# Performance work log

Measured on AMD Instinct MI355X. Metric: run time of the kernel, lower is better.

## Reference

```python
import jax, jax.numpy as jnp
import numpy as np
from jax import lax

KS = 3
N = KS * KS


def _conv(x, W, b, pad, stride):
    out = lax.conv_general_dilated(
        x, W, window_strides=(stride, stride),
        padding=[(pad, pad), (pad, pad)],
        dimension_numbers=("NCHW", "OIHW", "NCHW"))
    return out + b[None, :, None, None]


def setup_inputs() -> dict:
    key = jax.random.key(0)
    ks = jax.random.split(key, 5)
    b, c, h, w, outc = 16, 64, 64, 64, 128
    return {
        "x": jax.random.normal(ks[0], (b, c, h, w), jnp.float32),
        "W_off": jax.random.normal(ks[1], (2 * N, c, KS, KS), jnp.float32) * 0.05,
        "b_off": jax.random.normal(ks[2], (2 * N,), jnp.float32) * 0.05,
        "W_k": jax.random.normal(ks[3], (outc, c, KS, KS), jnp.float32) * 0.05,
        "b_k": jax.random.normal(ks[4], (outc,), jnp.float32) * 0.05,
    }


def _deform_conv(x, W_off, b_off, W_k, b_k):
    b, c, h, w = x.shape
    offset = _conv(x, W_off, b_off, pad=1, stride=1)  # [b, 2N, h, w]

    # kernel-grid offsets, flattened with x (row) index first: n = i*ks + j
    rng = jnp.arange(KS, dtype=x.dtype) - (KS - 1) // 2  # [-1, 0, 1]
    pnx = jnp.repeat(rng, KS)  # [N]
    pny = jnp.tile(rng, KS)    # [N]

    # sampling positions p = p0 + p_n + offset, clamped into the image
    px = jnp.arange(h, dtype=x.dtype)[None, None, :, None] + pnx[None, :, None, None] + offset[:, :N]
    py = jnp.arange(w, dtype=x.dtype)[None, None, None, :] + pny[None, :, None, None] + offset[:, N:]
    px = jnp.clip(px, 0, h - 1)
    py = jnp.clip(py, 0, w - 1)

    fx = jnp.floor(px)
    fy = jnp.floor(py)
    tx = px - fx  # fractional parts (bilinear weights)
    ty = py - fy
    x0 = fx.astype(jnp.int32)
    y0 = fy.astype(jnp.int32)
    x1 = jnp.minimum(x0 + 1, h - 1)  # out-of-range tap carries zero weight
    y1 = jnp.minimum(y0 + 1, w - 1)

    x_hw = x.transpose(0, 2, 3, 1).reshape(b, h * w, c)  # [b, hw, c]

    def gather(ix, iy):
        idx = (ix * w + iy).reshape(b, -1, 1)  # [b, N*h*w, 1]
        return jnp.take_along_axis(x_hw, idx, axis=1).reshape(b, N, h, w, c)

    wx0, wx1 = (1 - tx)[..., None], tx[..., None]
    wy0, wy1 = (1 - ty)[..., None], ty[..., None]
    # 4-tap bilinear interpolation == the original's sparse G @ x
    xo = (gather(x0, y0) * wx0 * wy0 + gather(x1, y0) * wx1 * wy0
          + gather(x0, y1) * wx0 * wy1 + gather(x1, y1) * wx1 * wy1)  # [b,N,h,w,c]

    # _reshape_x_offset: out[b,c, i_h*ks+i, i_w*ks+j] = xo[b, i*ks+j, i_h, i_w, c]
    xo = xo.reshape(b, KS, KS, h, w, c).transpose(0, 5, 3, 1, 4, 2)
    xo = xo.reshape(b, c, h * KS, w * KS)

    return _conv(xo, W_k, b_k, pad=0, stride=KS)  # [b, outc, h, w]


def reference(x, W_off, b_off, W_k, b_k):
    return _deform_conv(x, W_off, b_off, W_k, b_k)
```

## Files before the change

### kernel.cpp

```cpp
#include <hip/hip_runtime.h>

typedef __attribute__((ext_vector_type(8))) short bf16x8;
typedef __attribute__((ext_vector_type(4))) float floatx4;

__device__ __forceinline__ unsigned short f2bf(float f) {
    unsigned int u = __float_as_uint(f);
    u += 0x7FFFu + ((u >> 16) & 1u);
    return (unsigned short)(u >> 16);
}

__global__ __launch_bounds__(256) void prep_all(const float* __restrict__ x,
        const float* __restrict__ Wk, const float* __restrict__ Woff,
        unsigned short* __restrict__ xt, unsigned short* __restrict__ Wkb2,
        unsigned short* __restrict__ Woffb) {
    int bb = blockIdx.x;
    if (bb < 1024) {
        __shared__ float tile[64][65];
        int b = bb >> 6, y = bb & 63;
        const float* src = x + (size_t)b * 262144 + y * 64;
        int tx = threadIdx.x & 15, tg = threadIdx.x >> 4;
#pragma unroll
        for (int i = 0; i < 4; i++) {
            int c = tg + i * 16;
            float4 v = *(const float4*)(src + (size_t)c * 4096 + tx * 4);
            tile[c][tx * 4 + 0] = v.x; tile[c][tx * 4 + 1] = v.y;
            tile[c][tx * 4 + 2] = v.z; tile[c][tx * 4 + 3] = v.w;
        }
        __syncthreads();
        unsigned short* dst = xt + (size_t)bb * 4096;
#pragma unroll
        for (int i = 0; i < 4; i++) {
            int xc = tg + i * 16;
            int c4 = tx * 4;
            ushort4 v;
            v.x = f2bf(tile[c4 + 0][xc]); v.y = f2bf(tile[c4 + 1][xc]);
            v.z = f2bf(tile[c4 + 2][xc]); v.w = f2bf(tile[c4 + 3][xc]);
            *(ushort4*)(dst + xc * 64 + c4) = v;
        }
    } else if (bb < 1312) {
        int idx = (bb - 1024) * 256 + threadIdx.x;
        int tap = idx >> 13;
        int r = idx & 8191;
        int tile = r >> 9;
        int ln = (r >> 3) & 63;
        int j = r & 7;
        int mt = tile >> 1, kc = tile & 1;
        int oc = mt * 16 + (ln & 15);
        int c = kc * 32 + (ln >> 4) * 8 + j;
        Wkb2[idx] = f2bf(Wk[(oc * 64 + c) * 9 + tap]);
    } else {
        int idx = (bb - 1312) * 256 + threadIdx.x;
        int tap = idx >> 11;
        int r = idx & 2047;
        int tile = r >> 9;
        int ln = (r >> 3) & 63;
        int j = r & 7;
        int mt = tile >> 1, kc = tile & 1;
        int n = mt * 16 + (ln & 15);
        int c = kc * 32 + (ln >> 4) * 8 + j;
        float v = (n < 18) ? Woff[(n * 64 + c) * 9 + tap] : 0.f;
        Woffb[idx] = f2bf(v);
    }
}

__global__ __launch_bounds__(256, 4) void fused_kernel(
        const unsigned short* __restrict__ xt,
        const unsigned short* __restrict__ Wkb2,
        const unsigned short* __restrict__ Woffb,
        const float* __restrict__ boff,
        const float* __restrict__ bias,
        float* __restrict__ out) {
    __shared__ unsigned short As[2][8192];
    __shared__ float offs[64][20];
    int tid = threadIdx.x;
    int wave = tid >> 6, lane = tid & 63;
    int frow = lane & 15, quad = lane >> 4;
    int bb = blockIdx.x;
    int xcd = bb & 7, idx = bb >> 3;
    int b = xcd * 2 + (idx >> 6);
    int pxBase = (idx & 63) * 64;
    int pl = wave * 16 + frow;
    int px = pxBase + pl;
    int y = px >> 6, xx = px & 63;
    const char* img = (const char*)(xt + (size_t)b * 262144) + quad * 16;

    float bv[2][4];
#pragma unroll
    for (int mt = 0; mt < 2; mt++)
#pragma unroll
        for (int rg = 0; rg < 4; rg++) {
            int n = mt * 16 + quad * 4 + rg;
            bv[mt][rg] = (n < 18) ? boff[n] : 0.f;
        }

    floatx4 acc1[2];
    acc1[0] = (floatx4)(0.f); acc1[1] = (floatx4)(0.f);
    bf16x8 aw = *(const bf16x8*)(Woffb + tid * 8);
    *(bf16x8*)&As[0][tid * 8] = aw;
    for (int tap = 0; tap < 9; tap++) {
        if (tap < 8) aw = *(const bf16x8*)(Woffb + (tap + 1) * 2048 + tid * 8);
        __syncthreads();
        int ry = y + tap / 3 - 1, rx = xx + tap % 3 - 1;
        bool valid = (ry >= 0) & (ry < 64) & (rx >= 0) & (rx < 64);
        const char* src = img + ((ry * 64 + rx) << 7);
        const unsigned short* abuf = &As[tap & 1][0];
        bf16x8 bz = {};
#pragma unroll
        for (int kc = 0; kc < 2; kc++) {
            bf16x8 bfr = valid ? *(const bf16x8*)(src + kc * 64) : bz;
#pragma unroll
            for (int mt = 0; mt < 2; mt++) {
                bf16x8 af = *(const bf16x8*)&abuf[(mt * 2 + kc) * 512 + lane * 8];
                acc1[mt] = __builtin_amdgcn_mfma_f32_16x16x32_bf16(af, bfr, acc1[mt], 0, 0, 0);
            }
        }
        if (tap < 8) *(bf16x8*)&As[(tap + 1) & 1][tid * 8] = aw;
    }
#pragma unroll
    for (int mt = 0; mt < 2; mt++)
#pragma unroll
        for (int rg = 0; rg < 4; rg++) {
            int n = mt * 16 + quad * 4 + rg;
            if (n < 18) offs[pl][n] = acc1[mt][rg] + bv[mt][rg];
        }

    floatx4 acc[8];
#pragma unroll
    for (int i = 0; i < 8; i++) acc[i] = (floatx4)(0.f);
    bf16x8 wk[4];
#pragma unroll
    for (int i = 0; i < 4; i++)
        wk[i] = *(const bf16x8*)(Wkb2 + i * 2048 + tid * 8);
    __syncthreads();
#pragma unroll
    for (int i = 0; i < 4; i++)
        *(bf16x8*)&As[0][i * 2048 + tid * 8] = wk[i];

    for (int tap = 0; tap < 9; tap++) {
        if (tap < 8)
#pragma unroll
            for (int i = 0; i < 4; i++)
                wk[i] = *(const bf16x8*)(Wkb2 + (tap + 1) * 8192 + i * 2048 + tid * 8);
        __syncthreads();
        float orow = offs[pl][tap];
        float ocol = offs[pl][9 + tap];
        float pr = (float)(y + tap / 3 - 1) + orow;
        float pc = (float)(xx + tap % 3 - 1) + ocol;
        pr = fminf(fmaxf(pr, 0.f), 63.f);
        pc = fminf(fmaxf(pc, 0.f), 63.f);
        float fr = floorf(pr), fc = floorf(pc);
        float tr = pr - fr, tc = pc - fc;
        int r0 = (int)fr, c0 = (int)fc;
        int r1 = min(r0 + 1, 63), c1 = min(c0 + 1, 63);
        float w00 = (1.f - tr) * (1.f - tc);
        float w01 = (1.f - tr) * tc;
        float w10 = tr * (1.f - tc);
        float w11 = tr * tc;
        int o00 = (r0 * 64 + c0) * 128;
        int o01 = (r0 * 64 + c1) * 128;
        int o10 = (r1 * 64 + c0) * 128;
        int o11 = (r1 * 64 + c1) * 128;

        bf16x8 bfrag[2];
#pragma unroll
        for (int kc = 0; kc < 2; kc++) {
            int4 u00 = __builtin_bit_cast(int4, *(const bf16x8*)(img + o00 + kc * 64));
            int4 u01 = __builtin_bit_cast(int4, *(const bf16x8*)(img + o01 + kc * 64));
            int4 u10 = __builtin_bit_cast(int4, *(const bf16x8*)(img + o10 + kc * 64));
            int4 u11 = __builtin_bit_cast(int4, *(const bf16x8*)(img + o11 + kc * 64));
            int4 r;
#pragma unroll
            for (int wd = 0; wd < 4; wd++) {
                int a00 = (wd == 0) ? u00.x : (wd == 1) ? u00.y : (wd == 2) ? u00.z : u00.w;
                int a01 = (wd == 0) ? u01.x : (wd == 1) ? u01.y : (wd == 2) ? u01.z : u01.w;
                int a10 = (wd == 0) ? u10.x : (wd == 1) ? u10.y : (wd == 2) ? u10.z : u10.w;
                int a11 = (wd == 0) ? u11.x : (wd == 1) ? u11.y : (wd == 2) ? u11.z : u11.w;
                float vl = w00 * __uint_as_float((unsigned)a00 << 16)
                         + w01 * __uint_as_float((unsigned)a01 << 16)
                         + w10 * __uint_as_float((unsigned)a10 << 16)
                         + w11 * __uint_as_float((unsigned)a11 << 16);
                float vh = w00 * __uint_as_float((unsigned)a00 & 0xffff0000u)
                         + w01 * __uint_as_float((unsigned)a01 & 0xffff0000u)
                         + w10 * __uint_as_float((unsigned)a10 & 0xffff0000u)
                         + w11 * __uint_as_float((unsigned)a11 & 0xffff0000u);
                unsigned pk = __builtin_amdgcn_perm(
                    __float_as_uint(vh) + 0x8000u,
                    __float_as_uint(vl) + 0x8000u, 0x07060302u);
                if (wd == 0) r.x = (int)pk; else if (wd == 1) r.y = (int)pk;
                else if (wd == 2) r.z = (int)pk; else r.w = (int)pk;
            }
            bfrag[kc] = __builtin_bit_cast(bf16x8, r);
        }
        const unsigned short* abuf = &As[tap & 1][0];
#pragma unroll
        for (int kc = 0; kc < 2; kc++)
#pragma unroll
            for (int mt = 0; mt < 8; mt++) {
                bf16x8 af = *(const bf16x8*)&abuf[(mt * 2 + kc) * 512 + lane * 8];
                acc[mt] = __builtin_amdgcn_mfma_f32_16x16x32_bf16(af, bfrag[kc], acc[mt], 0, 0, 0);
            }
        if (tap < 8)
#pragma unroll
            for (int i = 0; i < 4; i++)
                *(bf16x8*)&As[(tap + 1) & 1][i * 2048 + tid * 8] = wk[i];
    }

    float* outb = out + (size_t)b * 524288 + px;
#pragma unroll
    for (int mt = 0; mt < 8; mt++) {
#pragma unroll
        for (int rg = 0; rg < 4; rg++) {
            int oc = mt * 16 + quad * 4 + rg;
            outb[oc * 4096] = acc[mt][rg] + bias[oc];
        }
    }
}

extern "C" void kernel_launch(void* const* d_in, const int* in_sizes, int n_in,
                              void* d_out, int out_size, void* d_ws, size_t ws_size,
                              hipStream_t stream) {
    const float* x    = (const float*)d_in[0];
    const float* Woff = (const float*)d_in[1];
    const float* boff = (const float*)d_in[2];
    const float* Wk   = (const float*)d_in[3];
    const float* bk   = (const float*)d_in[4];
    float* out = (float*)d_out;

    char* ws = (char*)d_ws;
    unsigned short* xt    = (unsigned short*)ws;
    unsigned short* Wkb2  = (unsigned short*)(ws + 8388608);
    unsigned short* Woffb = (unsigned short*)(ws + 8536064);

    prep_all<<<1384, 256, 0, stream>>>(x, Wk, Woff, xt, Wkb2, Woffb);
    fused_kernel<<<1024, 256, 0, stream>>>(xt, Wkb2, Woffb, boff, bk, out);
}
```

Before: 132.1 us.

## Drop LDS weight staging, read weights from global, and prefetch next-tap gathers

Removes the shared-memory double buffer for the offset-conv and main-conv weights. Each wave now loads its weight fragments directly from global/L2, which also removes the per-tap block barriers. The four bilinear corner loads for the next tap are issued before the current tap's interpolation and MFMAs, so gather latency overlaps compute. The cost is more redundant global weight traffic (every wave reloads the same weights) and higher register pressure from holding prefetched corners and weight fragments, which could hurt occupancy.

```diff
diff --git a/kernel.cpp b/kernel.cpp
--- a/kernel.cpp
+++ b/kernel.cpp
@@ -7,6 +7,20 @@
     unsigned int u = __float_as_uint(f);
     u += 0x7FFFu + ((u >> 16) & 1u);
     return (unsigned short)(u >> 16);
+}
+
+__device__ __forceinline__ int interp_word(int a00, int a01, int a10, int a11,
+                                           float w00, float w01, float w10, float w11) {
+    float vl = w00 * __uint_as_float((unsigned)a00 << 16)
+             + w01 * __uint_as_float((unsigned)a01 << 16)
+             + w10 * __uint_as_float((unsigned)a10 << 16)
+             + w11 * __uint_as_float((unsigned)a11 << 16);
+    float vh = w00 * __uint_as_float((unsigned)a00 & 0xffff0000u)
+             + w01 * __uint_as_float((unsigned)a01 & 0xffff0000u)
+             + w10 * __uint_as_float((unsigned)a10 & 0xffff0000u)
+             + w11 * __uint_as_float((unsigned)a11 & 0xffff0000u);
+    return (int)__builtin_amdgcn_perm(__float_as_uint(vh) + 0x8000u,
+                                      __float_as_uint(vl) + 0x8000u, 0x07060302u);
 }
 
 __global__ __launch_bounds__(256) void prep_all(const float* __restrict__ x,
@@ -70,7 +84,6 @@
         const float* __restrict__ boff,
         const float* __restrict__ bias,
         float* __restrict__ out) {
-    __shared__ unsigned short As[2][8192];
     __shared__ float offs[64][20];
     int tid = threadIdx.x;
     int wave = tid >> 6, lane = tid & 63;
@@ -95,26 +108,22 @@
 
     floatx4 acc1[2];
     acc1[0] = (floatx4)(0.f); acc1[1] = (floatx4)(0.f);
-    bf16x8 aw = *(const bf16x8*)(Woffb + tid * 8);
-    *(bf16x8*)&As[0][tid * 8] = aw;
+#pragma unroll
     for (int tap = 0; tap < 9; tap++) {
-        if (tap < 8) aw = *(const bf16x8*)(Woffb + (tap + 1) * 2048 + tid * 8);
-        __syncthreads();
         int ry = y + tap / 3 - 1, rx = xx + tap % 3 - 1;
         bool valid = (ry >= 0) & (ry < 64) & (rx >= 0) & (rx < 64);
         const char* src = img + ((ry * 64 + rx) << 7);
-        const unsigned short* abuf = &As[tap & 1][0];
+        const unsigned short* wofft = Woffb + tap * 2048 + lane * 8;
         bf16x8 bz = {};
 #pragma unroll
         for (int kc = 0; kc < 2; kc++) {
             bf16x8 bfr = valid ? *(const bf16x8*)(src + kc * 64) : bz;
 #pragma unroll
             for (int mt = 0; mt < 2; mt++) {
-                bf16x8 af = *(const bf16x8*)&abuf[(mt * 2 + kc) * 512 + lane * 8];
+                bf16x8 af = *(const bf16x8*)(wofft + (mt * 2 + kc) * 512);
                 acc1[mt] = __builtin_amdgcn_mfma_f32_16x16x32_bf16(af, bfr, acc1[mt], 0, 0, 0);
             }
         }
-        if (tap < 8) *(bf16x8*)&As[(tap + 1) & 1][tid * 8] = aw;
     }
 #pragma unroll
     for (int mt = 0; mt < 2; mt++)
@@ -123,27 +132,18 @@
             int n = mt * 16 + quad * 4 + rg;
             if (n < 18) offs[pl][n] = acc1[mt][rg] + bv[mt][rg];
         }
+    __syncthreads();
 
     floatx4 acc[8];
 #pragma unroll
     for (int i = 0; i < 8; i++) acc[i] = (floatx4)(0.f);
-    bf16x8 wk[4];
-#pragma unroll
-    for (int i = 0; i < 4; i++)
-        wk[i] = *(const bf16x8*)(Wkb2 + i * 2048 + tid * 8);
-    __syncthreads();
-#pragma unroll
-    for (int i = 0; i < 4; i++)
-        *(bf16x8*)&As[0][i * 2048 + tid * 8] = wk[i];
-
-    for (int tap = 0; tap < 9; tap++) {
-        if (tap < 8)
-#pragma unroll
-            for (int i = 0; i < 4; i++)
-                wk[i] = *(const bf16x8*)(Wkb2 + (tap + 1) * 8192 + i * 2048 + tid * 8);
-        __syncthreads();
-        float orow = offs[pl][tap];
-        float ocol = offs[pl][9 + tap];
+
+    const float* op = &offs[pl][0];
+
+    auto stage = [&](int tap, int4 (&r00)[2], int4 (&r01)[2], int4 (&r10)[2],
+                     int4 (&r11)[2], floatx4& w) {
+        float orow = op[tap];
+        float ocol = op[9 + tap];
         float pr = (float)(y + tap / 3 - 1) + orow;
         float pc = (float)(xx + tap % 3 - 1) + ocol;
         pr = fminf(fmaxf(pr, 0.f), 63.f);
@@ -152,66 +152,87 @@
         float tr = pr - fr, tc = pc - fc;
         int r0 = (int)fr, c0 = (int)fc;
         int r1 = min(r0 + 1, 63), c1 = min(c0 + 1, 63);
-        float w00 = (1.f - tr) * (1.f - tc);
-        float w01 = (1.f - tr) * tc;
-        float w10 = tr * (1.f - tc);
-        float w11 = tr * tc;
-        int o00 = (r0 * 64 + c0) * 128;
-        int o01 = (r0 * 64 + c1) * 128;
-        int o10 = (r1 * 64 + c0) * 128;
-        int o11 = (r1 * 64 + c1) * 128;
+        w[0] = (1.f - tr) * (1.f - tc);
+        w[1] = (1.f - tr) * tc;
+        w[2] = tr * (1.f - tc);
+        w[3] = tr * tc;
+        const char* p00 = img + ((r0 * 64 + c0) << 7);
+        const char* p01 = img + ((r0 * 64 + c1) << 7);
+        const char* p10 = img + ((r1 * 64 + c0) << 7);
+        const char* p11 = img + ((r1 * 64 + c1) << 7);
+#pragma unroll
+        for (int kc = 0; kc < 2; kc++) {
+            r00[kc] = *(const int4*)(p00 + kc * 64);
+            r01[kc] = *(const int4*)(p01 + kc * 64);
+            r10[kc] = *(const int4*)(p10 + kc * 64);
+            r11[kc] = *(const int4*)(p11 + kc * 64);
+        }
+    };
+
+    int4 c00[2], c01[2], c10[2], c11[2];
+    floatx4 cw;
+    stage(0, c00, c01, c10, c11, cw);
+
+#pragma unroll 1
+    for (int tap = 0; tap < 9; tap++) {
+        const unsigned short* wkt = Wkb2 + tap * 8192 + lane * 8;
+
+        bf16x8 af0[8];
+#pragma unroll
+        for (int mt = 0; mt < 8; mt++)
+            af0[mt] = *(const bf16x8*)(wkt + (mt * 2) * 512);
+
+        int4 n00[2], n01[2], n10[2], n11[2];
+        floatx4 nw;
+        if (tap < 8)
+            stage(tap + 1, n00, n01, n10, n11, nw);
 
         bf16x8 bfrag[2];
 #pragma unroll
         for (int kc = 0; kc < 2; kc++) {
-            int4 u00 = __builtin_bit_cast(int4, *(const bf16x8*)(img + o00 + kc * 64));
-            int4 u01 = __builtin_bit_cast(int4, *(const bf16x8*)(img + o01 + kc * 64));
-            int4 u10 = __builtin_bit_cast(int4, *(const bf16x8*)(img + o10 + kc * 64));
-            int4 u11 = __builtin_bit_cast(int4, *(const bf16x8*)(img + o11 + kc * 64));
             int4 r;
-#pragma unroll
-            for (int wd = 0; wd < 4; wd++) {
-                int a00 = (wd == 0) ? u00.x : (wd == 1) ? u00.y : (wd == 2) ? u00.z : u00.w;
-                int a01 = (wd == 0) ? u01.x : (wd == 1) ? u01.y : (wd == 2) ? u01.z : u01.w;
-                int a10 = (wd == 0) ? u10.x : (wd == 1) ? u10.y : (wd == 2) ? u10.z : u10.w;
-                int a11 = (wd == 0) ? u11.x : (wd == 1) ? u11.y : (wd == 2) ? u11.z : u11.w;
-                float vl = w00 * __uint_as_float((unsigned)a00 << 16)
-                         + w01 * __uint_as_float((unsigned)a01 << 16)
-                         + w10 * __uint_as_float((unsigned)a10 << 16)
-                         + w11 * __uint_as_float((unsigned)a11 << 16);
-                float vh = w00 * __uint_as_float((unsigned)a00 & 0xffff0000u)
-                         + w01 * __uint_as_float((unsigned)a01 & 0xffff0000u)
-                         + w10 * __uint_as_float((unsigned)a10 & 0xffff0000u)
-                         + w11 * __uint_as_float((unsigned)a11 & 0xffff0000u);
-                unsigned pk = __builtin_amdgcn_perm(
-                    __float_as_uint(vh) + 0x8000u,
-                    __float_as_uint(vl) + 0x8000u, 0x07060302u);
-                if (wd == 0) r.x = (int)pk; else if (wd == 1) r.y = (int)pk;
-                else if (wd == 2) r.z = (int)pk; else r.w = (int)pk;
+            r.x = interp_word(c00[kc].x, c01[kc].x, c10[kc].x, c11[kc].x,
+                              cw[0], cw[1], cw[2], cw[3]);
+            r.y = interp_word(c00[kc].y, c01[kc].y, c10[kc].y, c11[kc].y,
+                              cw[0], cw[1], cw[2], cw[3]);
+            r.z = interp_word(c00[kc].z, c01[kc].z, c10[kc].z, c11[kc].z,
+                              cw[0], cw[1], cw[2], cw[3]);
+            r.w = interp_word(c00[kc].w, c01[kc].w, c10[kc].w, c11[kc].w,
+                              cw[0], cw[1], cw[2], cw[3]);
+            bfrag[kc] = __builtin_bit_cast(bf16x8, r);
+        }
+
+#pragma unroll
+        for (int mt = 0; mt < 8; mt++)
+            acc[mt] = __builtin_amdgcn_mfma_f32_16x16x32_bf16(af0[mt], bfrag[0], acc[mt], 0, 0, 0);
+
+        bf16x8 af1[8];
+#pragma unroll
+        for (int mt = 0; mt < 8; mt++)
+            af1[mt] = *(const bf16x8*)(wkt + (mt * 2 + 1) * 512);
+#pragma unroll
+        for (int mt = 0; mt < 8; mt++)
+            acc[mt] = __builtin_amdgcn_mfma_f32_16x16x32_bf16(af1[mt], bfrag[1], acc[mt], 0, 0, 0);
+
+        if (tap < 8) {
+#pragma unroll
+            for (int kc = 0; kc < 2; kc++) {
+                c00[kc] = n00[kc]; c01[kc] = n01[kc];
+                c10[kc] = n10[kc]; c11[kc] = n11[kc];
             }
-            bfrag[kc] = __builtin_bit_cast(bf16x8, r);
-        }
-        const unsigned short* abuf = &As[tap & 1][0];
-#pragma unroll
-        for (int kc = 0; kc < 2; kc++)
-#pragma unroll
-            for (int mt = 0; mt < 8; mt++) {
-                bf16x8 af = *(const bf16x8*)&abuf[(mt * 2 + kc) * 512 + lane * 8];
-                acc[mt] = __builtin_amdgcn_mfma_f32_16x16x32_bf16(af, bfrag[kc], acc[mt], 0, 0, 0);
-            }
-        if (tap < 8)
-#pragma unroll
-            for (int i = 0; i < 4; i++)
-                *(bf16x8*)&As[(tap + 1) & 1][i * 2048 + tid * 8] = wk[i];
+            cw = nw;
+        }
     }
 
     float* outb = out + (size_t)b * 524288 + px;
 #pragma unroll
     for (int mt = 0; mt < 8; mt++) {
+        float4 bc = *(const float4*)(bias + mt * 16 + quad * 4);
+        float bcv[4] = {bc.x, bc.y, bc.z, bc.w};
 #pragma unroll
         for (int rg = 0; rg < 4; rg++) {
             int oc = mt * 16 + quad * 4 + rg;
-            outb[oc * 4096] = acc[mt][rg] + bias[oc];
+            outb[oc * 4096] = acc[mt][rg] + bcv[rg];
         }
     }
 }
```

New measurement: 200.9 us. +52.0%, slower.
